# Optimization experiments

Measured on AMD Instinct MI355X. Metric: run time of the kernel, lower is better.

## Reference

```python
import jax, jax.numpy as jnp
import numpy as np
import math

B, L, D_MODEL, D_HEAD = 4, 4096, 1024, 128

def setup_inputs() -> dict:
    key = jax.random.key(0)
    ks = jax.random.split(key, 9)
    s = 0.02
    return {
        "inp_q": jax.random.normal(ks[0], (B, L, D_MODEL), jnp.float32),
        "inp_k": jax.random.normal(ks[1], (B, L, D_MODEL), jnp.float32),
        "inp_v": jax.random.normal(ks[2], (B, L, D_MODEL), jnp.float32),
        "Wq": jax.random.normal(ks[3], (D_HEAD, D_MODEL), jnp.float32) * s,
        "bq": jax.random.normal(ks[4], (D_HEAD,), jnp.float32) * s,
        "Wk": jax.random.normal(ks[5], (D_HEAD, D_MODEL), jnp.float32) * s,
        "bk": jax.random.normal(ks[6], (D_HEAD,), jnp.float32) * s,
        "Wv": jax.random.normal(ks[7], (D_HEAD, D_MODEL), jnp.float32) * s,
        "bv": jax.random.normal(ks[8], (D_HEAD,), jnp.float32) * s,
    }

def reference(inp_q, inp_k, inp_v, Wq, bq, Wk, bk, Wv, bv):
    d_q = Wq.shape[0]
    # torch nn.Linear: y = x @ W.T + b
    Q = jnp.einsum('bld,qd->blq', inp_q, Wq) + bq   # [B, L, d_q]
    K = jnp.einsum('bld,kd->blk', inp_k, Wk) + bk   # [B, L, d_k]
    V = jnp.einsum('bld,vd->blv', inp_v, Wv) + bv   # [B, L, d_v]
    scores = jnp.einsum('bqe,bke->bqk', Q, K) / math.sqrt(d_q)  # [B, Lq, Lk]
    # NOTE: original uses nn.Softmax(dim=1) -> normalizes over the QUERY axis
    S = jax.nn.softmax(scores, axis=1)
    H = jnp.einsum('bqk,bkv->bqv', S, V)            # [B, Lq, d_v]
    return H
```

## Files before the change

### kernel.cpp

```cpp
#include <hip/hip_runtime.h>
#include <hip/hip_bf16.h>

#define B_  4
#define L_  4096
#define DM  1024
#define DH  128
#define KS  4
#define QS  4

#define SC2 0.12752844f

typedef __bf16 bf16_t;
typedef __attribute__((ext_vector_type(8))) __bf16 bf16x8;
typedef __attribute__((ext_vector_type(4))) __bf16 bf16x4;
typedef __attribute__((ext_vector_type(4))) float f32x4;

#if __has_builtin(__builtin_amdgcn_exp2f)
#define EXP2F(x) __builtin_amdgcn_exp2f(x)
#else
#define EXP2F(x) exp2f(x)
#endif

__device__ __forceinline__ f32x4 mfma16(bf16x8 a, bf16x8 b, f32x4 c) {
    return __builtin_amdgcn_mfma_f32_16x16x32_bf16(a, b, c, 0, 0, 0);
}

__device__ __forceinline__ int swz(int row, int rowbytes, int colbyte) {
    int slot = colbyte >> 4;
    return row * rowbytes + (((slot ^ (row & 7)) << 4) | (colbyte & 15));
}

__device__ __forceinline__ void gload_lds16(const void* g, void* l) {
    __builtin_amdgcn_global_load_lds((const __attribute__((address_space(1))) void*)g,
                                     (__attribute__((address_space(3))) void*)l, 16, 0, 0);
}

__global__ __launch_bounds__(256) void wcvt_kernel(
    const float* __restrict__ Wq, const float* __restrict__ Wk, const float* __restrict__ Wv,
    bf16_t* __restrict__ Wb)
{
    int idx = (blockIdx.x * 256 + threadIdx.x) * 8;
    int which = idx >> 17;
    int rem = idx & 131071;
    const float* W = which == 0 ? Wq : (which == 1 ? Wk : Wv);
    float4 a = *(const float4*)&W[rem];
    float4 b = *(const float4*)&W[rem + 4];
    bf16x8 o;
    o[0] = (__bf16)a.x; o[1] = (__bf16)a.y; o[2] = (__bf16)a.z; o[3] = (__bf16)a.w;
    o[4] = (__bf16)b.x; o[5] = (__bf16)b.y; o[6] = (__bf16)b.z; o[7] = (__bf16)b.w;
    *(bf16x8*)&Wb[idx] = o;
}

__device__ __forceinline__ void stage_w(
    const bf16_t* __restrict__ Wm, bf16_t* wb, int kt, int j, int lane, int wave)
{
    #pragma unroll
    for (int jj = 0; jj < 4; ++jj) {
        int c = wave * 4 + jj;
        int r = c * 8 + (lane >> 3);
        int s = lane & 7;
        gload_lds16(&Wm[(size_t)r * DM + kt * 256 + j * 64 + ((s ^ (r & 7)) << 3)],
                    (char*)wb + c * 1024);
    }
}

__global__ __launch_bounds__(256) void proj_kernel(
    const float* __restrict__ Xq, const float* __restrict__ Xk, const float* __restrict__ Xv,
    const bf16_t* __restrict__ Wb,
    const float* __restrict__ bq, const float* __restrict__ bk, const float* __restrict__ bv,
    bf16_t* __restrict__ Q, bf16_t* __restrict__ K, bf16_t* __restrict__ V)
{
    const int which = blockIdx.y;
    const float* X    = which == 0 ? Xq : (which == 1 ? Xk : Xv);
    const float* bias = which == 0 ? bq : (which == 1 ? bk : bv);
    bf16_t*      O    = which == 0 ? Q  : (which == 1 ? K  : V);
    const bf16_t* Wm  = Wb + (size_t)which * DH * DM;

    __shared__ bf16_t Xlds[64 * 256];
    __shared__ bf16_t Wlds[2][128 * 64];

    const int tid  = threadIdx.x;
    const int lane = tid & 63;
    const int wave = tid >> 6;
    const int wm = wave >> 1, wn = wave & 1;
    const int i16 = lane & 15, g4 = lane >> 4;
    const int l5  = lane >> 5, c32 = lane & 31;
    const int row0 = blockIdx.x * 64;

    f32x4 acc[2][4] = {};

    for (int kt = 0; kt < 4; ++kt) {
        __syncthreads();
        #pragma unroll
        for (int p = 0; p < 8; ++p) {
            int r = wave * 16 + p * 2 + l5;
            const float* g = &X[(size_t)(row0 + r) * DM + kt * 256 + c32 * 8];
            float4 a = *(const float4*)g;
            float4 b = *(const float4*)(g + 4);
            bf16x8 v;
            v[0] = (__bf16)a.x; v[1] = (__bf16)a.y; v[2] = (__bf16)a.z; v[3] = (__bf16)a.w;
            v[4] = (__bf16)b.x; v[5] = (__bf16)b.y; v[6] = (__bf16)b.z; v[7] = (__bf16)b.w;
            *(bf16x8*)((char*)Xlds + r * 512 + ((c32 ^ (r & 7)) << 4)) = v;
        }
        stage_w(Wm, Wlds[0], kt, 0, lane, wave);
        __syncthreads();

        #pragma unroll
        for (int j = 0; j < 4; ++j) {
            if (j < 3) stage_w(Wm, Wlds[(j + 1) & 1], kt, j + 1, lane, wave);
            const bf16_t* wb = Wlds[j & 1];
            #pragma unroll
            for (int ks = 0; ks < 2; ++ks) {
                int q = (j * 2 + ks) * 4 + g4;
                bf16x8 af[2], bfr[4];
                #pragma unroll
                for (int mi = 0; mi < 2; ++mi) {
                    int r = wm * 32 + mi * 16 + i16;
                    af[mi] = *(const bf16x8*)((const char*)Xlds + r * 512 + ((q ^ (r & 7)) << 4));
                }
                #pragma unroll
                for (int ni = 0; ni < 4; ++ni) {
                    int rw = wn * 64 + ni * 16 + i16;
                    int tt = ks * 4 + g4;
                    bfr[ni] = *(const bf16x8*)((const char*)wb + rw * 128 + ((tt ^ (rw & 7)) << 4));
                }
                #pragma unroll
                for (int mi = 0; mi < 2; ++mi)
                    #pragma unroll
                    for (int ni = 0; ni < 4; ++ni)
                        acc[mi][ni] = mfma16(af[mi], bfr[ni], acc[mi][ni]);
            }
            if (j < 3) {
                asm volatile("s_waitcnt vmcnt(0)" ::: "memory");
                __builtin_amdgcn_s_barrier();
            }
        }
    }

    #pragma unroll
    for (int ni = 0; ni < 4; ++ni) {
        int h = wn * 64 + ni * 16 + i16;
        float bb = bias[h];
        #pragma unroll
        for (int mi = 0; mi < 2; ++mi)
            #pragma unroll
            for (int j = 0; j < 4; ++j) {
                int r = row0 + wm * 32 + mi * 16 + g4 * 4 + j;
                O[(size_t)r * DH + h] = (__bf16)(acc[mi][ni][j] + bb);
            }
    }
}

__global__ __launch_bounds__(256) void stats_kernel(
    const bf16_t* __restrict__ Q, const bf16_t* __restrict__ K,
    float* __restrict__ Mpart, float* __restrict__ Lpart)
{
    const int b  = blockIdx.y;
    const int k0 = blockIdx.x * 64;
    const int qs = blockIdx.z;
    const int tid = threadIdx.x, lane = tid & 63, wave = tid >> 6;

    __shared__ bf16_t Klds[64 * 128];
    __shared__ bf16_t Qlds[128 * 128];

    const bf16_t* Kb = K + ((size_t)b * L_ + k0) * DH;
    #pragma unroll
    for (int it = 0; it < 4; ++it) {
        int id = it * 256 + tid;
        int r = id >> 4, s = id & 15;
        bf16x8 x = *(const bf16x8*)&Kb[(size_t)r * DH + s * 8];
        *(bf16x8*)((char*)Klds + swz(r, 256, s * 16)) = x;
    }
    __syncthreads();
    bf16x8 kfr[4][4];
    #pragma unroll
    for (int ni = 0; ni < 4; ++ni)
        #pragma unroll
        for (int ds = 0; ds < 4; ++ds) {
            int r = ni * 16 + (lane & 15);
            kfr[ni][ds] = *(const bf16x8*)((const char*)Klds + swz(r, 256, ds * 64 + (lane >> 4) * 16));
        }

    float mrun[4], lrun[4];
    #pragma unroll
    for (int ni = 0; ni < 4; ++ni) { mrun[ni] = -1e30f; lrun[ni] = 0.f; }

    const bf16_t* Qb = Q + (size_t)b * L_ * DH;
    const int qbase = qs * (L_ / QS);
    for (int q0 = qbase; q0 < qbase + L_ / QS; q0 += 128) {
        __syncthreads();
        #pragma unroll
        for (int it = 0; it < 8; ++it) {
            int id = it * 256 + tid;
            int r = id >> 4, s = id & 15;
            bf16x8 x = *(const bf16x8*)&Qb[(size_t)(q0 + r) * DH + s * 8];
            *(bf16x8*)((char*)Qlds + swz(r, 256, s * 16)) = x;
        }
        __syncthreads();
        f32x4 st[2][4] = {};
        #pragma unroll
        for (int mi = 0; mi < 2; ++mi)
            #pragma unroll
            for (int ds = 0; ds < 4; ++ds) {
                int r = wave * 32 + mi * 16 + (lane & 15);
                bf16x8 af = *(const bf16x8*)((const char*)Qlds + swz(r, 256, ds * 64 + (lane >> 4) * 16));
                #pragma unroll
                for (int ni = 0; ni < 4; ++ni)
                    st[mi][ni] = mfma16(af, kfr[ni][ds], st[mi][ni]);
            }
        #pragma unroll
        for (int ni = 0; ni < 4; ++ni) {
            float cm = -1e30f;
            #pragma unroll
            for (int mi = 0; mi < 2; ++mi)
                #pragma unroll
                for (int j = 0; j < 4; ++j) cm = fmaxf(cm, st[mi][ni][j]);
            cm *= SC2;
            cm = fmaxf(cm, __shfl_xor(cm, 16, 64));
            cm = fmaxf(cm, __shfl_xor(cm, 32, 64));
            float mnew = fmaxf(mrun[ni], cm);
            float p = 0.f;
            #pragma unroll
            for (int mi = 0; mi < 2; ++mi)
                #pragma unroll
                for (int j = 0; j < 4; ++j)
                    p += EXP2F(st[mi][ni][j] * SC2 - mnew);
            p += __shfl_xor(p, 16, 64);
            p += __shfl_xor(p, 32, 64);
            lrun[ni] = lrun[ni] * EXP2F(mrun[ni] - mnew) + p;
            mrun[ni] = mnew;
        }
    }
    __syncthreads();
    float* redm = (float*)Klds;
    float* redl = redm + 256;
    if (lane < 16) {
        #pragma unroll
        for (int ni = 0; ni < 4; ++ni) {
            redm[wave * 64 + ni * 16 + lane] = mrun[ni];
            redl[wave * 64 + ni * 16 + lane] = lrun[ni];
        }
    }
    __syncthreads();
    if (tid < 64) {
        float m0 = redm[tid], m1 = redm[64 + tid], m2v = redm[128 + tid], m3 = redm[192 + tid];
        float mt = fmaxf(fmaxf(m0, m1), fmaxf(m2v, m3));
        float lt = redl[tid]       * EXP2F(m0 - mt) + redl[64 + tid]  * EXP2F(m1 - mt)
                 + redl[128 + tid] * EXP2F(m2v - mt) + redl[192 + tid] * EXP2F(m3 - mt);
        Mpart[((size_t)qs * B_ + b) * L_ + k0 + tid] = mt;
        Lpart[((size_t)qs * B_ + b) * L_ + k0 + tid] = lt;
    }
}

__global__ __launch_bounds__(256) void comb_kernel(
    const float* __restrict__ Mpart, const float* __restrict__ Lpart,
    float* __restrict__ M2, float* __restrict__ Lsum)
{
    const size_t i = (size_t)blockIdx.x * 256 + threadIdx.x;
    const size_t N = (size_t)B_ * L_;
    float m = -1e30f;
    #pragma unroll
    for (int qs = 0; qs < QS; ++qs) m = fmaxf(m, Mpart[qs * N + i]);
    float l = 0.f;
    #pragma unroll
    for (int qs = 0; qs < QS; ++qs) l += Lpart[qs * N + i] * EXP2F(Mpart[qs * N + i] - m);
    M2[i] = m;
    Lsum[i] = l;
}

__global__ __launch_bounds__(256) void vt_kernel(
    const bf16_t* __restrict__ V, const float* __restrict__ Lsum, bf16_t* __restrict__ VT)
{
    const int b = blockIdx.z, v0 = blockIdx.y * 64, k0 = blockIdx.x * 64;
    __shared__ bf16_t tile[64][72];
    const int tid = threadIdx.x;
    const bf16_t* Vb = V + ((size_t)b * L_ + k0) * DH + v0;
    #pragma unroll
    for (int it = 0; it < 2; ++it) {
        int id = it * 256 + tid;
        int r = id >> 3, s = id & 7;
        bf16x8 x = *(const bf16x8*)&Vb[(size_t)r * DH + s * 8];
        *(bf16x8*)&tile[r][s * 8] = x;
    }
    __syncthreads();
    const int lane = tid & 63, wave = tid >> 6;
    float rl = 1.0f / Lsum[(size_t)b * L_ + k0 + lane];
    bf16_t* VTb = VT + ((size_t)b * DH + v0) * L_ + k0;
    #pragma unroll
    for (int i = 0; i < 16; ++i) {
        int v = wave * 16 + i;
        float x = (float)tile[lane][v];
        VTb[(size_t)v * L_ + lane] = (__bf16)(x * rl);
    }
}

__global__ __launch_bounds__(256) void pv_kernel(
    const bf16_t* __restrict__ Q, const bf16_t* __restrict__ K,
    const bf16_t* __restrict__ VT, const float* __restrict__ M2,
    float* __restrict__ out)
{
    const int b = blockIdx.y;
    const int q0 = blockIdx.x * 64;
    const int tid = threadIdx.x, lane = tid & 63, wave = tid >> 6;

    __shared__ bf16_t QPlds[64 * 128];
    __shared__ bf16_t Klds[64 * 128];
    __shared__ bf16_t VTlds[128 * 64];

    const bf16_t* Qb = Q + ((size_t)b * L_ + q0) * DH;
    #pragma unroll
    for (int it = 0; it < 4; ++it) {
        int id = it * 256 + tid;
        int r = id >> 4, s = id & 15;
        bf16x8 x = *(const bf16x8*)&Qb[(size_t)r * DH + s * 8];
        *(bf16x8*)((char*)QPlds + swz(r, 256, s * 16)) = x;
    }
    __syncthreads();
    bf16x8 qf[4][4];
    #pragma unroll
    for (int ni = 0; ni < 4; ++ni)
        #pragma unroll
        for (int ds = 0; ds < 4; ++ds) {
            int r = ni * 16 + (lane & 15);
            qf[ni][ds] = *(const bf16x8*)((const char*)QPlds + swz(r, 256, ds * 64 + (lane >> 4) * 16));
        }

    f32x4 acc[4][2] = {};
    const float*  m2b = M2 + (size_t)b * L_;
    const bf16_t* Kb  = K  + (size_t)b * L_ * DH;
    const bf16_t* VTb = VT + (size_t)b * DH * L_;
    bf16_t* Plds = QPlds;

    const int kbase = blockIdx.z * (L_ / KS);
    for (int kc = kbase; kc < kbase + L_ / KS; kc += 64) {
        __syncthreads();
        #pragma unroll
        for (int it = 0; it < 4; ++it) {
            int id = it * 256 + tid;
            int r = id >> 4, s = id & 15;
            bf16x8 x = *(const bf16x8*)&Kb[(size_t)(kc + r) * DH + s * 8];
            *(bf16x8*)((char*)Klds + swz(r, 256, s * 16)) = x;
        }
        #pragma unroll
        for (int it = 0; it < 4; ++it) {
            int id = it * 256 + tid;
            int r = id >> 3, s = id & 7;
            bf16x8 x = *(const bf16x8*)&VTb[(size_t)r * L_ + kc + s * 8];
            *(bf16x8*)((char*)VTlds + swz(r, 128, s * 16)) = x;
        }
        __syncthreads();
        f32x4 st[4] = {};
        #pragma unroll
        for (int ds = 0; ds < 4; ++ds) {
            int r = wave * 16 + (lane & 15);
            bf16x8 kf = *(const bf16x8*)((const char*)Klds + swz(r, 256, ds * 64 + (lane >> 4) * 16));
            #pragma unroll
            for (int ni = 0; ni < 4; ++ni)
                st[ni] = mfma16(kf, qf[ni][ds], st[ni]);
        }
        float4 mv = *(const float4*)&m2b[kc + wave * 16 + (lane >> 4) * 4];
        #pragma unroll
        for (int ni = 0; ni < 4; ++ni) {
            bf16x4 pk;
            pk[0] = (__bf16)EXP2F(st[ni][0] * SC2 - mv.x);
            pk[1] = (__bf16)EXP2F(st[ni][1] * SC2 - mv.y);
            pk[2] = (__bf16)EXP2F(st[ni][2] * SC2 - mv.z);
            pk[3] = (__bf16)EXP2F(st[ni][3] * SC2 - mv.w);
            int q = ni * 16 + (lane & 15);
            int colbyte = wave * 32 + (lane >> 4) * 8;
            *(bf16x4*)((char*)Plds + swz(q, 128, colbyte)) = pk;
        }
        __syncthreads();
        #pragma unroll
        for (int ks = 0; ks < 2; ++ks) {
            bf16x8 pf[4], vf[2];
            #pragma unroll
            for (int mi = 0; mi < 4; ++mi) {
                int q = mi * 16 + (lane & 15);
                pf[mi] = *(const bf16x8*)((const char*)Plds + swz(q, 128, ks * 64 + (lane >> 4) * 16));
            }
            #pragma unroll
            for (int ni = 0; ni < 2; ++ni) {
                int v = wave * 32 + ni * 16 + (lane & 15);
                vf[ni] = *(const bf16x8*)((const char*)VTlds + swz(v, 128, ks * 64 + (lane >> 4) * 16));
            }
            #pragma unroll
            for (int mi = 0; mi < 4; ++mi)
                #pragma unroll
                for (int ni = 0; ni < 2; ++ni)
                    acc[mi][ni] = mfma16(pf[mi], vf[ni], acc[mi][ni]);
        }
    }
    #pragma unroll
    for (int mi = 0; mi < 4; ++mi)
        #pragma unroll
        for (int ni = 0; ni < 2; ++ni)
            #pragma unroll
            for (int j = 0; j < 4; ++j) {
                int q = q0 + mi * 16 + (lane >> 4) * 4 + j;
                int v = wave * 32 + ni * 16 + (lane & 15);
                atomicAdd(&out[((size_t)b * L_ + q) * DH + v], acc[mi][ni][j]);
            }
}

extern "C" void kernel_launch(void* const* d_in, const int* in_sizes, int n_in,
                              void* d_out, int out_size, void* d_ws, size_t ws_size,
                              hipStream_t stream)
{
    const float* inq = (const float*)d_in[0];
    const float* ink = (const float*)d_in[1];
    const float* inv = (const float*)d_in[2];
    const float* Wq  = (const float*)d_in[3];
    const float* bq  = (const float*)d_in[4];
    const float* Wk  = (const float*)d_in[5];
    const float* bk  = (const float*)d_in[6];
    const float* Wv  = (const float*)d_in[7];
    const float* bv  = (const float*)d_in[8];
    float* out = (float*)d_out;

    const size_t nQKV = (size_t)B_ * L_ * DH;
    const size_t nBL  = (size_t)B_ * L_;
    char* ws = (char*)d_ws;
    bf16_t* Q  = (bf16_t*)ws;
    bf16_t* K  = Q + nQKV;
    bf16_t* V  = K + nQKV;
    bf16_t* VT = V + nQKV;
    float*  M2    = (float*)(VT + nQKV);
    float*  Lsum  = M2 + nBL;
    float*  Mpart = Lsum + nBL;
    float*  Lpart = Mpart + QS * nBL;
    bf16_t* Wbuf = VT;

    hipMemsetAsync(out, 0, nQKV * sizeof(float), stream);
    wcvt_kernel<<<dim3(192), 256, 0, stream>>>(Wq, Wk, Wv, Wbuf);
    proj_kernel<<<dim3(256, 3), 256, 0, stream>>>(inq, ink, inv, Wbuf, bq, bk, bv, Q, K, V);
    stats_kernel<<<dim3(L_ / 64, B_, QS), 256, 0, stream>>>(Q, K, Mpart, Lpart);
    comb_kernel<<<dim3(nBL / 256), 256, 0, stream>>>(Mpart, Lpart, M2, Lsum);
    vt_kernel<<<dim3(L_ / 64, DH / 64, B_), 256, 0, stream>>>(V, Lsum, VT);
    pv_kernel<<<dim3(L_ / 64, B_, KS), 256, 0, stream>>>(Q, K, VT, M2, out);
}
```

Before: 198.4 us.

## Split projection GEMM along reduction dim with atomics and raise attention split factors

Splits the QKV projection across four blocks along the model dimension. Each block loads its X slice once, reads W fragments directly from global memory, and atomically adds fp32 partials into new zeroed buffers. A separate kernel then adds the bias and converts the result to bf16. It also doubles the KS/QS split factors for the stats and PV kernels. The aim is more parallelism and shorter per-block work. The cost is an extra memset, fp32 atomic traffic, another kernel launch, and uncached W loads.

```diff
diff --git a/kernel.cpp b/kernel.cpp
--- a/kernel.cpp
+++ b/kernel.cpp
@@ -5,8 +5,8 @@
 #define L_  4096
 #define DM  1024
 #define DH  128
-#define KS  4
-#define QS  4
+#define KS  8
+#define QS  8
 
 #define SC2 0.12752844f
 
@@ -28,11 +28,6 @@
 __device__ __forceinline__ int swz(int row, int rowbytes, int colbyte) {
     int slot = colbyte >> 4;
     return row * rowbytes + (((slot ^ (row & 7)) << 4) | (colbyte & 15));
-}
-
-__device__ __forceinline__ void gload_lds16(const void* g, void* l) {
-    __builtin_amdgcn_global_load_lds((const __attribute__((address_space(1))) void*)g,
-                                     (__attribute__((address_space(3))) void*)l, 16, 0, 0);
 }
 
 __global__ __launch_bounds__(256) void wcvt_kernel(
@@ -51,33 +46,17 @@
     *(bf16x8*)&Wb[idx] = o;
 }
 
-__device__ __forceinline__ void stage_w(
-    const bf16_t* __restrict__ Wm, bf16_t* wb, int kt, int j, int lane, int wave)
-{
-    #pragma unroll
-    for (int jj = 0; jj < 4; ++jj) {
-        int c = wave * 4 + jj;
-        int r = c * 8 + (lane >> 3);
-        int s = lane & 7;
-        gload_lds16(&Wm[(size_t)r * DM + kt * 256 + j * 64 + ((s ^ (r & 7)) << 3)],
-                    (char*)wb + c * 1024);
-    }
-}
-
-__global__ __launch_bounds__(256) void proj_kernel(
+__global__ __launch_bounds__(256) void projk_kernel(
     const float* __restrict__ Xq, const float* __restrict__ Xk, const float* __restrict__ Xv,
     const bf16_t* __restrict__ Wb,
-    const float* __restrict__ bq, const float* __restrict__ bk, const float* __restrict__ bv,
-    bf16_t* __restrict__ Q, bf16_t* __restrict__ K, bf16_t* __restrict__ V)
+    float* __restrict__ Qf, float* __restrict__ Kf, float* __restrict__ Vf)
 {
     const int which = blockIdx.y;
-    const float* X    = which == 0 ? Xq : (which == 1 ? Xk : Xv);
-    const float* bias = which == 0 ? bq : (which == 1 ? bk : bv);
-    bf16_t*      O    = which == 0 ? Q  : (which == 1 ? K  : V);
-    const bf16_t* Wm  = Wb + (size_t)which * DH * DM;
+    const float* X = which == 0 ? Xq : (which == 1 ? Xk : Xv);
+    float*       Of = which == 0 ? Qf : (which == 1 ? Kf : Vf);
+    const bf16_t* Wm = Wb + (size_t)which * DH * DM;
 
     __shared__ bf16_t Xlds[64 * 256];
-    __shared__ bf16_t Wlds[2][128 * 64];
 
     const int tid  = threadIdx.x;
     const int lane = tid & 63;
@@ -86,69 +65,81 @@
     const int i16 = lane & 15, g4 = lane >> 4;
     const int l5  = lane >> 5, c32 = lane & 31;
     const int row0 = blockIdx.x * 64;
+    const int kz   = blockIdx.z;
+
+    #pragma unroll
+    for (int p = 0; p < 8; ++p) {
+        int r = wave * 16 + p * 2 + l5;
+        const float* g = &X[(size_t)(row0 + r) * DM + kz * 256 + c32 * 8];
+        float4 a = *(const float4*)g;
+        float4 b = *(const float4*)(g + 4);
+        bf16x8 v;
+        v[0] = (__bf16)a.x; v[1] = (__bf16)a.y; v[2] = (__bf16)a.z; v[3] = (__bf16)a.w;
+        v[4] = (__bf16)b.x; v[5] = (__bf16)b.y; v[6] = (__bf16)b.z; v[7] = (__bf16)b.w;
+        *(bf16x8*)((char*)Xlds + r * 512 + ((c32 ^ (r & 7)) << 4)) = v;
+    }
+    __syncthreads();
 
     f32x4 acc[2][4] = {};
-
-    for (int kt = 0; kt < 4; ++kt) {
-        __syncthreads();
-        #pragma unroll
-        for (int p = 0; p < 8; ++p) {
-            int r = wave * 16 + p * 2 + l5;
-            const float* g = &X[(size_t)(row0 + r) * DM + kt * 256 + c32 * 8];
-            float4 a = *(const float4*)g;
-            float4 b = *(const float4*)(g + 4);
-            bf16x8 v;
-            v[0] = (__bf16)a.x; v[1] = (__bf16)a.y; v[2] = (__bf16)a.z; v[3] = (__bf16)a.w;
-            v[4] = (__bf16)b.x; v[5] = (__bf16)b.y; v[6] = (__bf16)b.z; v[7] = (__bf16)b.w;
-            *(bf16x8*)((char*)Xlds + r * 512 + ((c32 ^ (r & 7)) << 4)) = v;
-        }
-        stage_w(Wm, Wlds[0], kt, 0, lane, wave);
-        __syncthreads();
-
-        #pragma unroll
-        for (int j = 0; j < 4; ++j) {
-            if (j < 3) stage_w(Wm, Wlds[(j + 1) & 1], kt, j + 1, lane, wave);
-            const bf16_t* wb = Wlds[j & 1];
-            #pragma unroll
-            for (int ks = 0; ks < 2; ++ks) {
-                int q = (j * 2 + ks) * 4 + g4;
-                bf16x8 af[2], bfr[4];
+    #pragma unroll
+    for (int j = 0; j < 4; ++j) {
+        #pragma unroll
+        for (int ks = 0; ks < 2; ++ks) {
+            int q = (j * 2 + ks) * 4 + g4;
+            bf16x8 af[2], bfr[4];
+            #pragma unroll
+            for (int mi = 0; mi < 2; ++mi) {
+                int r = wm * 32 + mi * 16 + i16;
+                af[mi] = *(const bf16x8*)((const char*)Xlds + r * 512 + ((q ^ (r & 7)) << 4));
+            }
+            #pragma unroll
+            for (int ni = 0; ni < 4; ++ni) {
+                int rw = wn * 64 + ni * 16 + i16;
+                bfr[ni] = *(const bf16x8*)&Wm[(size_t)rw * DM + kz * 256 + j * 64 + ks * 32 + g4 * 8];
+            }
+            #pragma unroll
+            for (int mi = 0; mi < 2; ++mi)
                 #pragma unroll
-                for (int mi = 0; mi < 2; ++mi) {
-                    int r = wm * 32 + mi * 16 + i16;
-                    af[mi] = *(const bf16x8*)((const char*)Xlds + r * 512 + ((q ^ (r & 7)) << 4));
-                }
-                #pragma unroll
-                for (int ni = 0; ni < 4; ++ni) {
-                    int rw = wn * 64 + ni * 16 + i16;
-                    int tt = ks * 4 + g4;
-                    bfr[ni] = *(const bf16x8*)((const char*)wb + rw * 128 + ((tt ^ (rw & 7)) << 4));
-                }
-                #pragma unroll
-                for (int mi = 0; mi < 2; ++mi)
-                    #pragma unroll
-                    for (int ni = 0; ni < 4; ++ni)
-                        acc[mi][ni] = mfma16(af[mi], bfr[ni], acc[mi][ni]);
-            }
-            if (j < 3) {
-                asm volatile("s_waitcnt vmcnt(0)" ::: "memory");
-                __builtin_amdgcn_s_barrier();
-            }
+                for (int ni = 0; ni < 4; ++ni)
+                    acc[mi][ni] = mfma16(af[mi], bfr[ni], acc[mi][ni]);
         }
     }
 
     #pragma unroll
     for (int ni = 0; ni < 4; ++ni) {
         int h = wn * 64 + ni * 16 + i16;
-        float bb = bias[h];
         #pragma unroll
         for (int mi = 0; mi < 2; ++mi)
             #pragma unroll
-            for (int j = 0; j < 4; ++j) {
-                int r = row0 + wm * 32 + mi * 16 + g4 * 4 + j;
-                O[(size_t)r * DH + h] = (__bf16)(acc[mi][ni][j] + bb);
-            }
-    }
+            for (int jj = 0; jj < 4; ++jj) {
+                int r = row0 + wm * 32 + mi * 16 + g4 * 4 + jj;
+                atomicAdd(&Of[(size_t)r * DH + h], acc[mi][ni][jj]);
+            }
+    }
+}
+
+__global__ __launch_bounds__(256) void cvtbias_kernel(
+    const float* __restrict__ Qf, const float* __restrict__ Kf, const float* __restrict__ Vf,
+    const float* __restrict__ bq, const float* __restrict__ bk, const float* __restrict__ bv,
+    bf16_t* __restrict__ Q, bf16_t* __restrict__ K, bf16_t* __restrict__ V)
+{
+    size_t f8 = ((size_t)blockIdx.x * 256 + threadIdx.x) * 8;
+    int which = (int)(f8 >> 21);
+    size_t rem = f8 & ((1u << 21) - 1);
+    const float* Of   = which == 0 ? Qf : (which == 1 ? Kf : Vf);
+    const float* bias = which == 0 ? bq : (which == 1 ? bk : bv);
+    bf16_t*      O    = which == 0 ? Q  : (which == 1 ? K  : V);
+    int h0 = (int)(rem & 127);
+    float4 p0 = *(const float4*)&Of[rem];
+    float4 p1 = *(const float4*)&Of[rem + 4];
+    float4 b0 = *(const float4*)&bias[h0];
+    float4 b1 = *(const float4*)&bias[h0 + 4];
+    bf16x8 o;
+    o[0] = (__bf16)(p0.x + b0.x); o[1] = (__bf16)(p0.y + b0.y);
+    o[2] = (__bf16)(p0.z + b0.z); o[3] = (__bf16)(p0.w + b0.w);
+    o[4] = (__bf16)(p1.x + b1.x); o[5] = (__bf16)(p1.y + b1.y);
+    o[6] = (__bf16)(p1.z + b1.z); o[7] = (__bf16)(p1.w + b1.w);
+    *(bf16x8*)&O[rem] = o;
 }
 
 __global__ __launch_bounds__(256) void stats_kernel(
@@ -429,11 +420,16 @@
     float*  Lsum  = M2 + nBL;
     float*  Mpart = Lsum + nBL;
     float*  Lpart = Mpart + QS * nBL;
+    float*  Qf    = Lpart + QS * nBL;
+    float*  Kf    = Qf + nQKV;
+    float*  Vf    = Kf + nQKV;
     bf16_t* Wbuf = VT;
 
     hipMemsetAsync(out, 0, nQKV * sizeof(float), stream);
+    hipMemsetAsync(Qf, 0, 3 * nQKV * sizeof(float), stream);
     wcvt_kernel<<<dim3(192), 256, 0, stream>>>(Wq, Wk, Wv, Wbuf);
-    proj_kernel<<<dim3(256, 3), 256, 0, stream>>>(inq, ink, inv, Wbuf, bq, bk, bv, Q, K, V);
+    projk_kernel<<<dim3(256, 3, 4), 256, 0, stream>>>(inq, ink, inv, Wbuf, Qf, Kf, Vf);
+    cvtbias_kernel<<<dim3(3072), 256, 0, stream>>>(Qf, Kf, Vf, bq, bk, bv, Q, K, V);
     stats_kernel<<<dim3(L_ / 64, B_, QS), 256, 0, stream>>>(Q, K, Mpart, Lpart);
     comb_kernel<<<dim3(nBL / 256), 256, 0, stream>>>(Mpart, Lpart, M2, Lsum);
     vt_kernel<<<dim3(L_ / 64, DH / 64, B_), 256, 0, stream>>>(V, Lsum, VT);
```

Result: slower. 268.0 us (+35.1%).

## Restructure projection to stage full 32-row X tile and raise split factors

Applied to the files above, without the earlier changes.

The projection kernel now converts a whole 32x1024 row block of X to bf16 in LDS once, then streams W in 64-column chunks over 16 steps. Each wave computes a 32x32 output tile, and the grid doubles to 512 blocks per matrix. The KS and QS split factors are raised from 4 to 8, so the stats and PV kernels get more parallel blocks at the cost of more partial results to combine. The single-buffered W staging with two barriers per step removes the earlier double-buffer overlap, and the 64 KB X tile limits how many blocks fit per CU.

```diff
diff --git a/kernel.cpp b/kernel.cpp
--- a/kernel.cpp
+++ b/kernel.cpp
@@ -5,8 +5,8 @@
 #define L_  4096
 #define DM  1024
 #define DH  128
-#define KS  4
-#define QS  4
+#define KS  8
+#define QS  8
 
 #define SC2 0.12752844f
 
@@ -30,6 +30,13 @@
     return row * rowbytes + (((slot ^ (row & 7)) << 4) | (colbyte & 15));
 }
 
+__device__ __forceinline__ bf16x8 cvt8v(f32x4 a, f32x4 b) {
+    bf16x8 v;
+    v[0] = (__bf16)a.x; v[1] = (__bf16)a.y; v[2] = (__bf16)a.z; v[3] = (__bf16)a.w;
+    v[4] = (__bf16)b.x; v[5] = (__bf16)b.y; v[6] = (__bf16)b.z; v[7] = (__bf16)b.w;
+    return v;
+}
+
 __device__ __forceinline__ void gload_lds16(const void* g, void* l) {
     __builtin_amdgcn_global_load_lds((const __attribute__((address_space(1))) void*)g,
                                      (__attribute__((address_space(3))) void*)l, 16, 0, 0);
@@ -43,28 +50,12 @@
     int which = idx >> 17;
     int rem = idx & 131071;
     const float* W = which == 0 ? Wq : (which == 1 ? Wk : Wv);
-    float4 a = *(const float4*)&W[rem];
-    float4 b = *(const float4*)&W[rem + 4];
-    bf16x8 o;
-    o[0] = (__bf16)a.x; o[1] = (__bf16)a.y; o[2] = (__bf16)a.z; o[3] = (__bf16)a.w;
-    o[4] = (__bf16)b.x; o[5] = (__bf16)b.y; o[6] = (__bf16)b.z; o[7] = (__bf16)b.w;
-    *(bf16x8*)&Wb[idx] = o;
-}
-
-__device__ __forceinline__ void stage_w(
-    const bf16_t* __restrict__ Wm, bf16_t* wb, int kt, int j, int lane, int wave)
-{
-    #pragma unroll
-    for (int jj = 0; jj < 4; ++jj) {
-        int c = wave * 4 + jj;
-        int r = c * 8 + (lane >> 3);
-        int s = lane & 7;
-        gload_lds16(&Wm[(size_t)r * DM + kt * 256 + j * 64 + ((s ^ (r & 7)) << 3)],
-                    (char*)wb + c * 1024);
-    }
-}
-
-__global__ __launch_bounds__(256) void proj_kernel(
+    f32x4 a = *(const f32x4*)&W[rem];
+    f32x4 b = *(const f32x4*)&W[rem + 4];
+    *(bf16x8*)&Wb[idx] = cvt8v(a, b);
+}
+
+__global__ __launch_bounds__(256) void projc_kernel(
     const float* __restrict__ Xq, const float* __restrict__ Xk, const float* __restrict__ Xv,
     const bf16_t* __restrict__ Wb,
     const float* __restrict__ bq, const float* __restrict__ bk, const float* __restrict__ bv,
@@ -76,76 +67,74 @@
     bf16_t*      O    = which == 0 ? Q  : (which == 1 ? K  : V);
     const bf16_t* Wm  = Wb + (size_t)which * DH * DM;
 
-    __shared__ bf16_t Xlds[64 * 256];
-    __shared__ bf16_t Wlds[2][128 * 64];
+    __shared__ bf16_t Xp[32 * 1024];
+    __shared__ bf16_t Wc[128 * 64];
 
     const int tid  = threadIdx.x;
     const int lane = tid & 63;
     const int wave = tid >> 6;
-    const int wm = wave >> 1, wn = wave & 1;
     const int i16 = lane & 15, g4 = lane >> 4;
-    const int l5  = lane >> 5, c32 = lane & 31;
-    const int row0 = blockIdx.x * 64;
-
-    f32x4 acc[2][4] = {};
-
-    for (int kt = 0; kt < 4; ++kt) {
-        __syncthreads();
-        #pragma unroll
-        for (int p = 0; p < 8; ++p) {
-            int r = wave * 16 + p * 2 + l5;
-            const float* g = &X[(size_t)(row0 + r) * DM + kt * 256 + c32 * 8];
-            float4 a = *(const float4*)g;
-            float4 b = *(const float4*)(g + 4);
-            bf16x8 v;
-            v[0] = (__bf16)a.x; v[1] = (__bf16)a.y; v[2] = (__bf16)a.z; v[3] = (__bf16)a.w;
-            v[4] = (__bf16)b.x; v[5] = (__bf16)b.y; v[6] = (__bf16)b.z; v[7] = (__bf16)b.w;
-            *(bf16x8*)((char*)Xlds + r * 512 + ((c32 ^ (r & 7)) << 4)) = v;
-        }
-        stage_w(Wm, Wlds[0], kt, 0, lane, wave);
-        __syncthreads();
-
+    const int row0 = blockIdx.x * 32;
+
+    #pragma unroll
+    for (int p = 0; p < 8; ++p) {
+        int r = wave * 8 + p;
+        const float* rowp = &X[(size_t)(row0 + r) * DM];
+        #pragma unroll
+        for (int h = 0; h < 2; ++h) {
+            f32x4 a = *(const f32x4*)&rowp[h * 512 + lane * 8];
+            f32x4 b = *(const f32x4*)&rowp[h * 512 + lane * 8 + 4];
+            int s = h * 64 + lane;
+            *(bf16x8*)((char*)Xp + r * 2048 + ((s ^ (r & 7)) << 4)) = cvt8v(a, b);
+        }
+    }
+
+    f32x4 acc[2][2] = {};
+
+    for (int t = 0; t < 16; ++t) {
         #pragma unroll
         for (int j = 0; j < 4; ++j) {
-            if (j < 3) stage_w(Wm, Wlds[(j + 1) & 1], kt, j + 1, lane, wave);
-            const bf16_t* wb = Wlds[j & 1];
-            #pragma unroll
-            for (int ks = 0; ks < 2; ++ks) {
-                int q = (j * 2 + ks) * 4 + g4;
-                bf16x8 af[2], bfr[4];
+            int c = j * 4 + wave;
+            int r = c * 8 + (lane >> 3);
+            int s = lane & 7;
+            gload_lds16(&Wm[(size_t)r * DM + t * 64 + ((s ^ (r & 7)) << 3)],
+                        (char*)Wc + c * 1024);
+        }
+        __syncthreads();
+
+        #pragma unroll
+        for (int ks = 0; ks < 2; ++ks) {
+            int q = t * 8 + ks * 4 + g4;
+            bf16x8 af[2], wf[2];
+            #pragma unroll
+            for (int mi = 0; mi < 2; ++mi) {
+                int r = mi * 16 + i16;
+                af[mi] = *(const bf16x8*)((const char*)Xp + r * 2048 + ((q ^ (r & 7)) << 4));
+            }
+            #pragma unroll
+            for (int ni = 0; ni < 2; ++ni) {
+                int rw = wave * 32 + ni * 16 + i16;
+                int tt = ks * 4 + g4;
+                wf[ni] = *(const bf16x8*)((const char*)Wc + rw * 128 + ((tt ^ (rw & 7)) << 4));
+            }
+            #pragma unroll
+            for (int mi = 0; mi < 2; ++mi)
                 #pragma unroll
-                for (int mi = 0; mi < 2; ++mi) {
-                    int r = wm * 32 + mi * 16 + i16;
-                    af[mi] = *(const bf16x8*)((const char*)Xlds + r * 512 + ((q ^ (r & 7)) << 4));
-                }
-                #pragma unroll
-                for (int ni = 0; ni < 4; ++ni) {
-                    int rw = wn * 64 + ni * 16 + i16;
-                    int tt = ks * 4 + g4;
-                    bfr[ni] = *(const bf16x8*)((const char*)wb + rw * 128 + ((tt ^ (rw & 7)) << 4));
-                }
-                #pragma unroll
-                for (int mi = 0; mi < 2; ++mi)
-                    #pragma unroll
-                    for (int ni = 0; ni < 4; ++ni)
-                        acc[mi][ni] = mfma16(af[mi], bfr[ni], acc[mi][ni]);
-            }
-            if (j < 3) {
-                asm volatile("s_waitcnt vmcnt(0)" ::: "memory");
-                __builtin_amdgcn_s_barrier();
-            }
-        }
-    }
-
-    #pragma unroll
-    for (int ni = 0; ni < 4; ++ni) {
-        int h = wn * 64 + ni * 16 + i16;
+                for (int ni = 0; ni < 2; ++ni)
+                    acc[mi][ni] = mfma16(af[mi], wf[ni], acc[mi][ni]);
+        }
+        __syncthreads();
+    }
+
+    #pragma unroll
+    for (int ni = 0; ni < 2; ++ni) {
+        int h = wave * 32 + ni * 16 + i16;
         float bb = bias[h];
         #pragma unroll
         for (int mi = 0; mi < 2; ++mi)
             #pragma unroll
             for (int j = 0; j < 4; ++j) {
-                int r = row0 + wm * 32 + mi * 16 + g4 * 4 + j;
+                int r = row0 + mi * 16 + g4 * 4 + j;
                 O[(size_t)r * DH + h] = (__bf16)(acc[mi][ni][j] + bb);
             }
     }
@@ -358,7 +347,7 @@
             for (int ni = 0; ni < 4; ++ni)
                 st[ni] = mfma16(kf, qf[ni][ds], st[ni]);
         }
-        float4 mv = *(const float4*)&m2b[kc + wave * 16 + (lane >> 4) * 4];
+        f32x4 mv = *(const f32x4*)&m2b[kc + wave * 16 + (lane >> 4) * 4];
         #pragma unroll
         for (int ni = 0; ni < 4; ++ni) {
             bf16x4 pk;
@@ -431,9 +420,9 @@
     float*  Lpart = Mpart + QS * nBL;
     bf16_t* Wbuf = VT;
 
-    hipMemsetAsync(out, 0, nQKV * sizeof(float), stream);
+    (void)hipMemsetAsync(out, 0, nQKV * sizeof(float), stream);
     wcvt_kernel<<<dim3(192), 256, 0, stream>>>(Wq, Wk, Wv, Wbuf);
-    proj_kernel<<<dim3(256, 3), 256, 0, stream>>>(inq, ink, inv, Wbuf, bq, bk, bv, Q, K, V);
+    projc_kernel<<<dim3(512, 3), 256, 0, stream>>>(inq, ink, inv, Wbuf, bq, bk, bv, Q, K, V);
     stats_kernel<<<dim3(L_ / 64, B_, QS), 256, 0, stream>>>(Q, K, Mpart, Lpart);
     comb_kernel<<<dim3(nBL / 256), 256, 0, stream>>>(Mpart, Lpart, M2, Lsum);
     vt_kernel<<<dim3(L_ / 64, DH / 64, B_), 256, 0, stream>>>(V, Lsum, VT);
```

Result: faster. 185.2 us (-6.7%).
